# Performance work log

Hardware: AMD Instinct MI355X
Metric: run time of the kernel (lower is better)

Reference implementation:

```python
import jax, jax.numpy as jnp
import numpy as np

D_MODEL = 2048
NUM_HEADS = 16
D_K = D_MODEL // NUM_HEADS
THETA = 10000.0
MAX_SEQ_LEN = 2048
GPT_INIT_STD = 0.02


def setup_inputs() -> dict:
    key = jax.random.key(0)
    ks = jax.random.split(key, 5)
    B, T = 4, 2048
    x = jax.random.normal(ks[0], (B, T, D_MODEL), dtype=jnp.float32)
    token_positions = jnp.arange(T, dtype=jnp.int64 if jax.config.jax_enable_x64 else jnp.int32)[None, :]
    Wq = jax.random.normal(ks[1], (D_MODEL, D_MODEL), dtype=jnp.float32) * GPT_INIT_STD
    Wk = jax.random.normal(ks[2], (D_MODEL, D_MODEL), dtype=jnp.float32) * GPT_INIT_STD
    Wv = jax.random.normal(ks[3], (D_MODEL, D_MODEL), dtype=jnp.float32) * GPT_INIT_STD
    Wo = jax.random.normal(ks[4], (D_MODEL, D_MODEL), dtype=jnp.float32) * GPT_INIT_STD
    return {"x": x, "token_positions": token_positions, "Wq": Wq, "Wk": Wk, "Wv": Wv, "Wo": Wo}


def _rope_tables(dtype):
    # angles[p, j] = p * theta^(-2j/d_k), j in [0, d_k/2)
    j = jnp.arange(D_K // 2, dtype=jnp.float32)
    inv_freq = THETA ** (-2.0 * j / float(D_K))
    pos = jnp.arange(MAX_SEQ_LEN, dtype=jnp.float32)[:, None]
    angles = pos * inv_freq[None, :]
    return jnp.cos(angles).astype(dtype), jnp.sin(angles).astype(dtype)


def _apply_rope(t, cos_pos, sin_pos):
    # t: (b, h, s, d); cos/sin: (1, s, d/2) -> broadcast over (b, h)
    even = t[..., 0::2]
    odd = t[..., 1::2]
    c = cos_pos[:, None, :, :]  # (1,1,s,d/2)
    s = sin_pos[:, None, :, :]
    rot_even = even * c - odd * s
    rot_odd = even * s + odd * c
    out = jnp.stack([rot_even, rot_odd], axis=-1)  # (b,h,s,d/2,2)
    return out.reshape(t.shape)


def reference(x, token_positions, Wq, Wk, Wv, Wo):
    B, T, D = x.shape
    H, d = NUM_HEADS, D_K
    q = (x @ Wq.T).reshape(B, T, H, d).transpose(0, 2, 1, 3)  # (b,h,t,d)
    k = (x @ Wk.T).reshape(B, T, H, d).transpose(0, 2, 1, 3)
    v = (x @ Wv.T).reshape(B, T, H, d).transpose(0, 2, 1, 3)

    cos_tab, sin_tab = _rope_tables(x.dtype)
    cos_pos = cos_tab[token_positions]  # (1, t, d/2)
    sin_pos = sin_tab[token_positions]
    q = _apply_rope(q, cos_pos, sin_pos)
    k = _apply_rope(k, cos_pos, sin_pos)

    # token_positions is strictly increasing and attention_mask is None,
    # so build_attention_mask returns None -> unmasked eager attention.
    scale = float(d) ** -0.5
    scores = jnp.einsum('bhtd,bhsd->bhts', q, k) * scale
    attn = jax.nn.softmax(scores.astype(jnp.float32), axis=-1).astype(q.dtype)
    out = jnp.einsum('bhts,bhsd->bhtd', attn, v)  # (b,h,t,d)
    out = out.transpose(0, 2, 1, 3).reshape(B, T, D)  # (b,t,h*d)
    return out @ Wo.T
```

## Files before the change

kernel.cpp:

```cpp
#include <hip/hip_runtime.h>
#include <hip/hip_bf16.h>
#include <math.h>

#define TSEQ   2048
#define DMODEL 2048
#define NHEAD  16
#define DHEAD  128
#define NBATCH 4
#define MROWS  (NBATCH*TSEQ)

typedef __attribute__((ext_vector_type(8))) short v8s;
typedef __attribute__((ext_vector_type(4))) float v4f;
typedef __attribute__((ext_vector_type(16))) float v16f;

#if __has_builtin(__builtin_amdgcn_exp2f)
#define EXP2(x) __builtin_amdgcn_exp2f(x)
#else
#define EXP2(x) __expf((x) * 0.6931471805599453f)
#endif

__device__ __forceinline__ unsigned short f2b(float f) {
  __hip_bfloat16 h = __float2bfloat16(f);
  return *reinterpret_cast<unsigned short*>(&h);
}
__device__ __forceinline__ unsigned int cvtpk(float lo, float hi) {
  unsigned int r;
  asm("v_cvt_pk_bf16_f32 %0, %1, %2" : "=v"(r) : "v"(lo), "v"(hi));
  return r;
}
__device__ __forceinline__ void gload_lds16(const unsigned short* g, unsigned short* l) {
  __builtin_amdgcn_global_load_lds(
      (const __attribute__((address_space(1))) unsigned int*)g,
      (__attribute__((address_space(3))) unsigned int*)l, 16, 0, 0);
}

__global__ void prep_kernel(const float* __restrict__ x,  const float* __restrict__ Wq,
                            const float* __restrict__ Wk, const float* __restrict__ Wv,
                            const float* __restrict__ Wo, const int* __restrict__ pos,
                            unsigned short* __restrict__ xb,  unsigned short* __restrict__ wqb,
                            unsigned short* __restrict__ wkb, unsigned short* __restrict__ wvb,
                            unsigned short* __restrict__ wob,
                            float* __restrict__ cosT, float* __restrict__ sinT) {
  const int blk = blockIdx.x, tid = threadIdx.x;
  if (blk < 32768) {
    const float* in; unsigned short* out; int lb;
    if      (blk < 16384) { in = x;  out = xb;  lb = blk; }
    else if (blk < 20480) { in = Wq; out = wqb; lb = blk - 16384; }
    else if (blk < 24576) { in = Wk; out = wkb; lb = blk - 20480; }
    else if (blk < 28672) { in = Wv; out = wvb; lb = blk - 24576; }
    else                  { in = Wo; out = wob; lb = blk - 28672; }
    int i = lb * 256 + tid;
    float4 v = reinterpret_cast<const float4*>(in)[i];
    ushort4 o;
    o.x = f2b(v.x); o.y = f2b(v.y); o.z = f2b(v.z); o.w = f2b(v.w);
    reinterpret_cast<ushort4*>(out)[i] = o;
  } else {
    int idx = (blk - 32768) * 256 + tid;
    int t = idx >> 6, j = idx & 63;
    float p = (float)pos[t];
    float inv_freq = expf((-2.0f * (float)j / 128.0f) * logf(10000.0f));
    float ang = p * inv_freq;
    cosT[idx] = cosf(ang);
    sinT[idx] = sinf(ang);
  }
}

template<int MODE>
__global__ __launch_bounds__(512, 2) void gemm8(const unsigned short* __restrict__ A,
                                                const unsigned short* __restrict__ Bt,
                                                void* __restrict__ Cout,
                                                const float* __restrict__ cosT,
                                                const float* __restrict__ sinT) {
  __shared__ unsigned short ldsA[2][256 * 64];
  __shared__ unsigned short ldsB[2][256 * 64];
  const int tid = threadIdx.x;
  const int lane = tid & 63, wv = tid >> 6;
  const int wr = wv >> 2, wc = wv & 3;
  const int g = lane >> 4, r16 = lane & 15;
  const int r7 = r16 & 7;
  const int sl0 = (g ^ r7) << 3;
  const int sl1 = ((4 + g) ^ r7) << 3;

  const int nx = gridDim.x;
  const int nwg = nx * gridDim.y;
  const int lid = blockIdx.y * nx + blockIdx.x;
  const int q8 = nwg >> 3, r8 = nwg & 7;
  const int xcd = lid & 7, off = lid >> 3;
  const int nlid = (xcd < r8 ? xcd * (q8 + 1) : r8 * (q8 + 1) + (xcd - r8) * q8) + off;
  const int mrow0 = (nlid / nx) * 256;
  const int ncol0 = (nlid % nx) * 256;

  const int srow = tid >> 3;
  const int sslot = tid & 7;

  auto stA = [&](int kt, int b, int hf) {
    const int k0 = kt * 64;
#pragma unroll
    for (int j = 0; j < 2; ++j) {
      int r = hf * 128 + j * 64 + srow;
      int slot = sslot ^ (r & 7);
      gload_lds16(&A[(size_t)(mrow0 + r) * DMODEL + k0 + slot * 8],
                  &ldsA[b][(hf * 128 + j * 64) * 64 + tid * 8]);
    }
  };
  auto stB = [&](int kt, int b, int hf) {
    const int k0 = kt * 64;
#pragma unroll
    for (int j = 0; j < 2; ++j) {
      int r = hf * 128 + j * 64 + srow;
      int slot = sslot ^ (r & 7);
      gload_lds16(&Bt[(size_t)(ncol0 + r) * DMODEL + k0 + slot * 8],
                  &ldsB[b][(hf * 128 + j * 64) * 64 + tid * 8]);
    }
  };

  v4f zero = {0.f, 0.f, 0.f, 0.f};
  v4f acc[8][4];
#pragma unroll
  for (int m = 0; m < 8; ++m)
#pragma unroll
    for (int n = 0; n < 4; ++n) acc[m][n] = zero;

  stA(0, 0, 0); stA(0, 0, 1); stB(0, 0, 0); stB(0, 0, 1);
  stA(1, 1, 0); stA(1, 1, 1); stB(1, 1, 0); stB(1, 1, 1);
  asm volatile("s_waitcnt vmcnt(8)" ::: "memory");
  __builtin_amdgcn_s_barrier();

  v8s af[4][2], bf[4][2];
  const int arow = wr * 128 + r16;
  const int brow = wc * 64 + r16;

  for (int kt = 0; kt < DMODEL / 64; ++kt) {
    const int p = kt & 1;
    unsigned short* LA = ldsA[p];
    unsigned short* LB = ldsB[p];

#pragma unroll
    for (int m = 0; m < 4; ++m) {
      af[m][0] = *(const v8s*)&LA[(arow + m * 16) * 64 + sl0];
      af[m][1] = *(const v8s*)&LA[(arow + m * 16) * 64 + sl1];
    }
#pragma unroll
    for (int n = 0; n < 2; ++n) {
      bf[n][0] = *(const v8s*)&LB[(brow + n * 16) * 64 + sl0];
      bf[n][1] = *(const v8s*)&LB[(brow + n * 16) * 64 + sl1];
    }
    __builtin_amdgcn_s_barrier();
    asm volatile("s_waitcnt lgkmcnt(0)" ::: "memory");
    __builtin_amdgcn_sched_barrier(0);
    __builtin_amdgcn_s_setprio(1);
#pragma unroll
    for (int m = 0; m < 4; ++m)
#pragma unroll
      for (int n = 0; n < 2; ++n) {
        acc[m][n] = __builtin_amdgcn_mfma_f32_16x16x32_bf16(af[m][0], bf[n][0], acc[m][n], 0, 0, 0);
        acc[m][n] = __builtin_amdgcn_mfma_f32_16x16x32_bf16(af[m][1], bf[n][1], acc[m][n], 0, 0, 0);
      }
    __builtin_amdgcn_s_setprio(0);
    __builtin_amdgcn_s_barrier();

#pragma unroll
    for (int n = 2; n < 4; ++n) {
      bf[n][0] = *(const v8s*)&LB[(brow + n * 16) * 64 + sl0];
      bf[n][1] = *(const v8s*)&LB[(brow + n * 16) * 64 + sl1];
    }
    __builtin_amdgcn_s_barrier();
    asm volatile("s_waitcnt lgkmcnt(0)" ::: "memory");
    __builtin_amdgcn_sched_barrier(0);
    __builtin_amdgcn_s_setprio(1);
#pragma unroll
    for (int m = 0; m < 4; ++m)
#pragma unroll
      for (int n = 2; n < 4; ++n) {
        acc[m][n] = __builtin_amdgcn_mfma_f32_16x16x32_bf16(af[m][0], bf[n][0], acc[m][n], 0, 0, 0);
        acc[m][n] = __builtin_amdgcn_mfma_f32_16x16x32_bf16(af[m][1], bf[n][1], acc[m][n], 0, 0, 0);
      }
    __builtin_amdgcn_s_setprio(0);
    __builtin_amdgcn_s_barrier();

#pragma unroll
    for (int m = 0; m < 4; ++m) {
      af[m][0] = *(const v8s*)&LA[(arow + 64 + m * 16) * 64 + sl0];
      af[m][1] = *(const v8s*)&LA[(arow + 64 + m * 16) * 64 + sl1];
    }
    if (kt < DMODEL / 64 - 2) { stB(kt + 2, p, 0); stB(kt + 2, p, 1); }
    __builtin_amdgcn_s_barrier();
    asm volatile("s_waitcnt lgkmcnt(0)" ::: "memory");
    __builtin_amdgcn_sched_barrier(0);
    __builtin_amdgcn_s_setprio(1);
#pragma unroll
    for (int m = 0; m < 4; ++m)
#pragma unroll
      for (int n = 2; n < 4; ++n) {
        acc[m + 4][n] = __builtin_amdgcn_mfma_f32_16x16x32_bf16(af[m][0], bf[n][0], acc[m + 4][n], 0, 0, 0);
        acc[m + 4][n] = __builtin_amdgcn_mfma_f32_16x16x32_bf16(af[m][1], bf[n][1], acc[m + 4][n], 0, 0, 0);
      }
    __builtin_amdgcn_s_setprio(0);
    __builtin_amdgcn_s_barrier();

    if (kt < DMODEL / 64 - 2) {
      stA(kt + 2, p, 0); stA(kt + 2, p, 1);
      asm volatile("s_waitcnt vmcnt(8)" ::: "memory");
    } else {
      asm volatile("s_waitcnt vmcnt(0)" ::: "memory");
    }
    __builtin_amdgcn_s_barrier();
    __builtin_amdgcn_s_setprio(1);
#pragma unroll
    for (int m = 0; m < 4; ++m)
#pragma unroll
      for (int n = 0; n < 2; ++n) {
        acc[m + 4][n] = __builtin_amdgcn_mfma_f32_16x16x32_bf16(af[m][0], bf[n][0], acc[m + 4][n], 0, 0, 0);
        acc[m + 4][n] = __builtin_amdgcn_mfma_f32_16x16x32_bf16(af[m][1], bf[n][1], acc[m + 4][n], 0, 0, 0);
      }
    __builtin_amdgcn_s_setprio(0);
    __builtin_amdgcn_s_barrier();
  }

#pragma unroll
  for (int m = 0; m < 8; ++m) {
#pragma unroll
    for (int n = 0; n < 4; ++n) {
#pragma unroll
      for (int r = 0; r < 4; ++r) {
        int row = mrow0 + wr * 128 + m * 16 + g * 4 + r;
        int col = ncol0 + wc * 64 + n * 16 + r16;
        float val = acc[m][n][r];
        if (MODE <= 1) {
          int t = row & (TSEQ - 1), bb = row >> 11;
          int hh = col >> 7, dd = col & (DHEAD - 1);
          float c = cosT[(t << 6) + (dd >> 1)];
          float s = sinT[(t << 6) + (dd >> 1)];
          float pv = __shfl_xor(val, 1);
          float rot = (r16 & 1) ? (pv * s + val * c) : (val * c - pv * s);
          if (MODE == 0) rot *= 0.12751726f;
          ((unsigned short*)Cout)[(((size_t)bb * NHEAD + hh) * TSEQ + t) * DHEAD + dd] = f2b(rot);
        } else if (MODE == 2) {
          int hh = row >> 7, dd = row & (DHEAD - 1);
          int bb = col >> 11, tt = col & (TSEQ - 1);
          ((unsigned short*)Cout)[(((size_t)bb * NHEAD + hh) * DHEAD + dd) * TSEQ + tt] = f2b(val);
        } else {
          ((float*)Cout)[(size_t)row * DMODEL + col] = val;
        }
      }
    }
  }
}

__global__ __launch_bounds__(256, 2) void attn_kernel(const unsigned short* __restrict__ Q,
                                                      const unsigned short* __restrict__ K,
                                                      const unsigned short* __restrict__ Vt,
                                                      unsigned short* __restrict__ O) {
  __shared__ unsigned short Ks[64 * 128];
  __shared__ unsigned short Vs[128 * 64];
  const int tid = threadIdx.x, lane = tid & 63, w = tid >> 6;
  const int hi = lane >> 5, l31 = lane & 31;
  const int bh = blockIdx.y;
  const int b = bh >> 4, h = bh & 15;
  const int qbase = blockIdx.x * 128;
  const size_t hb = (size_t)bh * TSEQ * DHEAD;
  const size_t vb = (size_t)bh * DHEAD * TSEQ;

  v8s qf[8];
  {
    const int qrow = qbase + w * 32 + l31;
#pragma unroll
    for (int dk = 0; dk < 8; ++dk)
      qf[dk] = *(const v8s*)&Q[hb + (size_t)qrow * DHEAD + dk * 16 + hi * 8];
  }

  v16f Z16 = {0,0,0,0,0,0,0,0,0,0,0,0,0,0,0,0};
  v16f o_acc[4];
#pragma unroll
  for (int d = 0; d < 4; ++d) o_acc[d] = Z16;
  float l_run = 0.0f;

  const int ck0 = tid;
  v8s kst[4], vst[4];

#pragma unroll
  for (int hh = 0; hh < 4; ++hh) {
    int ck = ck0 + hh * 256;
    kst[hh] = *(const v8s*)&K[hb + (size_t)(ck >> 4) * DHEAD + (ck & 15) * 8];
    vst[hh] = *(const v8s*)&Vt[vb + (size_t)(ck >> 3) * TSEQ + (ck & 7) * 8];
  }
#pragma unroll
  for (int hh = 0; hh < 4; ++hh) {
    int ck = ck0 + hh * 256;
    int kr = ck >> 4, kc = (ck & 15) * 8;
    *(v8s*)&Ks[kr * 128 + (kc ^ ((kr & 15) << 3))] = kst[hh];
    int vr = ck >> 3, vg = ck & 7;
    *(v8s*)&Vs[vr * 64 + (((vg ^ (vr & 7))) << 3)] = vst[hh];
  }
  __syncthreads();

  for (int s0 = 0; s0 < TSEQ; s0 += 64) {
    const bool last = (s0 + 64 >= TSEQ);
    if (!last) {
#pragma unroll
      for (int hh = 0; hh < 4; ++hh) {
        int ck = ck0 + hh * 256;
        kst[hh] = *(const v8s*)&K[hb + (size_t)(s0 + 64 + (ck >> 4)) * DHEAD + (ck & 15) * 8];
      }
#pragma unroll
      for (int hh = 0; hh < 4; ++hh) {
        int ck = ck0 + hh * 256;
        vst[hh] = *(const v8s*)&Vt[vb + (size_t)(ck >> 3) * TSEQ + s0 + 64 + (ck & 7) * 8];
      }
    }

    v16f s[2]; s[0] = Z16; s[1] = Z16;
    __builtin_amdgcn_s_setprio(1);
#pragma unroll
    for (int kvt = 0; kvt < 2; ++kvt) {
#pragma unroll
      for (int dk = 0; dk < 8; ++dk) {
        int krow = kvt * 32 + l31;
        v8s a = *(const v8s*)&Ks[krow * 128 + ((dk * 16 + hi * 8) ^ ((krow & 15) << 3))];
        s[kvt] = __builtin_amdgcn_mfma_f32_32x32x16_bf16(a, qf[dk], s[kvt], 0, 0, 0);
      }
    }
    __builtin_amdgcn_s_setprio(0);

    __syncthreads();

    if (!last) {
#pragma unroll
      for (int hh = 0; hh < 4; ++hh) {
        int ck = ck0 + hh * 256;
        int kr = ck >> 4, kc = (ck & 15) * 8;
        *(v8s*)&Ks[kr * 128 + (kc ^ ((kr & 15) << 3))] = kst[hh];
      }
    }

    float rowsum = 0.f;
#pragma unroll
    for (int kvt = 0; kvt < 2; ++kvt)
#pragma unroll
      for (int r = 0; r < 16; ++r) {
        float pp = EXP2(s[kvt][r]);
        s[kvt][r] = pp; rowsum += pp;
      }
    l_run += rowsum;

    union { unsigned int u[4]; v8s v; } pf[4];
#pragma unroll
    for (int kvt = 0; kvt < 2; ++kvt) {
      unsigned int wpk[8];
#pragma unroll
      for (int i = 0; i < 8; ++i) wpk[i] = cvtpk(s[kvt][2 * i], s[kvt][2 * i + 1]);
      asm("v_permlane32_swap_b32 %0, %1" : "+v"(wpk[0]), "+v"(wpk[2]));
      asm("v_permlane32_swap_b32 %0, %1" : "+v"(wpk[1]), "+v"(wpk[3]));
      asm("v_permlane32_swap_b32 %0, %1" : "+v"(wpk[4]), "+v"(wpk[6]));
      asm("v_permlane32_swap_b32 %0, %1" : "+v"(wpk[5]), "+v"(wpk[7]));
      pf[2 * kvt].u[0] = wpk[0]; pf[2 * kvt].u[1] = wpk[1];
      pf[2 * kvt].u[2] = wpk[2]; pf[2 * kvt].u[3] = wpk[3];
      pf[2 * kvt + 1].u[0] = wpk[4]; pf[2 * kvt + 1].u[1] = wpk[5];
      pf[2 * kvt + 1].u[2] = wpk[6]; pf[2 * kvt + 1].u[3] = wpk[7];
    }

    __builtin_amdgcn_s_setprio(1);
#pragma unroll
    for (int kvt = 0; kvt < 2; ++kvt) {
      const int g0 = kvt * 4 + hi;
#pragma unroll
      for (int d = 0; d < 4; ++d) {
        int drow = d * 32 + l31;
        int sx = drow & 7;
        v8s vf0 = *(const v8s*)&Vs[drow * 64 + (((g0    ) ^ sx) << 3)];
        v8s vf1 = *(const v8s*)&Vs[drow * 64 + (((g0 + 2) ^ sx) << 3)];
        o_acc[d] = __builtin_amdgcn_mfma_f32_32x32x16_bf16(pf[2 * kvt].v, vf0, o_acc[d], 0, 0, 0);
        o_acc[d] = __builtin_amdgcn_mfma_f32_32x32x16_bf16(pf[2 * kvt + 1].v, vf1, o_acc[d], 0, 0, 0);
      }
    }
    __builtin_amdgcn_s_setprio(0);

    __syncthreads();

    if (!last) {
#pragma unroll
      for (int hh = 0; hh < 4; ++hh) {
        int ck = ck0 + hh * 256;
        int vr = ck >> 3, vg = ck & 7;
        *(v8s*)&Vs[vr * 64 + (((vg ^ (vr & 7))) << 3)] = vst[hh];
      }
    }
  }

#pragma unroll
  for (int r = 0; r < 16; ++r) {
    int qi = (r & 3) + 8 * (r >> 2) + 4 * hi;
    float lq = __shfl(l_run, qi) + __shfl(l_run, qi + 32);
    float inv = 1.0f / lq;
    int t = qbase + w * 32 + qi;
#pragma unroll
    for (int d = 0; d < 4; ++d) {
      O[((size_t)(b * TSEQ + t)) * DMODEL + h * DHEAD + d * 32 + l31] = f2b(o_acc[d][r] * inv);
    }
  }
}

extern "C" void kernel_launch(void* const* d_in, const int* in_sizes, int n_in,
                              void* d_out, int out_size, void* d_ws, size_t ws_size,
                              hipStream_t stream) {
  const float* x  = (const float*)d_in[0];
  const int*   pos = (const int*)d_in[1];
  const float* Wq = (const float*)d_in[2];
  const float* Wk = (const float*)d_in[3];
  const float* Wv = (const float*)d_in[4];
  const float* Wo = (const float*)d_in[5];
  float* out = (float*)d_out;
  char* ws = (char*)d_ws;

  const size_t WBYTES = (size_t)DMODEL * DMODEL * 2;
  const size_t XBYTES = (size_t)MROWS * DMODEL * 2;
  unsigned short* wqb = (unsigned short*)(ws);
  unsigned short* wkb = (unsigned short*)(ws + WBYTES);
  unsigned short* wvb = (unsigned short*)(ws + 2 * WBYTES);
  unsigned short* wob = (unsigned short*)(ws + 3 * WBYTES);
  unsigned short* xb  = (unsigned short*)(ws + 4 * WBYTES);
  unsigned short* Qb  = (unsigned short*)(ws + 4 * WBYTES + XBYTES);
  unsigned short* Kb  = (unsigned short*)(ws + 4 * WBYTES + 2 * XBYTES);
  unsigned short* Vtb = (unsigned short*)(ws + 4 * WBYTES + 3 * XBYTES);
  float* cosT = (float*)(ws + 4 * WBYTES + 4 * XBYTES);
  float* sinT = cosT + TSEQ * 64;
  if (ws_size < 4 * WBYTES + 4 * XBYTES + 2 * (size_t)TSEQ * 64 * sizeof(float)) return;

  prep_kernel<<<33280, 256, 0, stream>>>(x, Wq, Wk, Wv, Wo, pos,
                                         xb, wqb, wkb, wvb, wob, cosT, sinT);

  dim3 gg(DMODEL / 256, MROWS / 256);
  gemm8<0><<<gg, 512, 0, stream>>>(xb, wqb, (void*)Qb, cosT, sinT);
  gemm8<1><<<gg, 512, 0, stream>>>(xb, wkb, (void*)Kb, cosT, sinT);
  gemm8<2><<<dim3(MROWS / 256, DMODEL / 256), 512, 0, stream>>>(wvb, xb, (void*)Vtb, cosT, sinT);

  attn_kernel<<<dim3(TSEQ / 128, 64), 256, 0, stream>>>(Qb, Kb, Vtb, xb);

  gemm8<3><<<gg, 512, 0, stream>>>(xb, wob, (void*)out, cosT, sinT);
}
```

Before: 485.1 us.

## Pack RoPE cos/sin as fp16 pairs and reswizzle V tile in attention LDS

The RoPE tables are now stored as one interleaved half2 word per (position, frequency) instead of two separate float arrays, so the projection epilogue does a single 4-byte load per element. This lowers epilogue memory traffic but reduces cos/sin precision to fp16. Separately, the V tile in the attention kernel's LDS is laid out as 128-wide rows, two d-rows per row, with a 16-way XOR swizzle. The aim is to cut LDS bank conflicts on the V fragment reads feeding the MFMAs.

```diff
diff --git a/kernel.cpp b/kernel.cpp
--- a/kernel.cpp
+++ b/kernel.cpp
@@ -1,5 +1,6 @@
 #include <hip/hip_runtime.h>
 #include <hip/hip_bf16.h>
+#include <hip/hip_fp16.h>
 #include <math.h>
 
 #define TSEQ   2048
@@ -40,7 +41,7 @@
                             unsigned short* __restrict__ xb,  unsigned short* __restrict__ wqb,
                             unsigned short* __restrict__ wkb, unsigned short* __restrict__ wvb,
                             unsigned short* __restrict__ wob,
-                            float* __restrict__ cosT, float* __restrict__ sinT) {
+                            unsigned int* __restrict__ ropeT) {
   const int blk = blockIdx.x, tid = threadIdx.x;
   if (blk < 32768) {
     const float* in; unsigned short* out; int lb;
@@ -60,8 +61,8 @@
     float p = (float)pos[t];
     float inv_freq = expf((-2.0f * (float)j / 128.0f) * logf(10000.0f));
     float ang = p * inv_freq;
-    cosT[idx] = cosf(ang);
-    sinT[idx] = sinf(ang);
+    __half2 h2 = __floats2half2_rn(cosf(ang), sinf(ang));
+    ropeT[idx] = *reinterpret_cast<unsigned int*>(&h2);
   }
 }
 
@@ -69,8 +70,7 @@
 __global__ __launch_bounds__(512, 2) void gemm8(const unsigned short* __restrict__ A,
                                                 const unsigned short* __restrict__ Bt,
                                                 void* __restrict__ Cout,
-                                                const float* __restrict__ cosT,
-                                                const float* __restrict__ sinT) {
+                                                const unsigned int* __restrict__ ropeT) {
   __shared__ unsigned short ldsA[2][256 * 64];
   __shared__ unsigned short ldsB[2][256 * 64];
   const int tid = threadIdx.x;
@@ -229,8 +229,10 @@
         if (MODE <= 1) {
           int t = row & (TSEQ - 1), bb = row >> 11;
           int hh = col >> 7, dd = col & (DHEAD - 1);
-          float c = cosT[(t << 6) + (dd >> 1)];
-          float s = sinT[(t << 6) + (dd >> 1)];
+          unsigned int csu = ropeT[(t << 6) + (dd >> 1)];
+          __half2 h2 = *reinterpret_cast<__half2*>(&csu);
+          float c = __half2float(__low2half(h2));
+          float s = __half2float(__high2half(h2));
           float pv = __shfl_xor(val, 1);
           float rot = (r16 & 1) ? (pv * s + val * c) : (val * c - pv * s);
           if (MODE == 0) rot *= 0.12751726f;
@@ -252,7 +254,7 @@
                                                       const unsigned short* __restrict__ Vt,
                                                       unsigned short* __restrict__ O) {
   __shared__ unsigned short Ks[64 * 128];
-  __shared__ unsigned short Vs[128 * 64];
+  __shared__ unsigned short Vs[64 * 128];
   const int tid = threadIdx.x, lane = tid & 63, w = tid >> 6;
   const int hi = lane >> 5, l31 = lane & 31;
   const int bh = blockIdx.y;
@@ -290,7 +292,8 @@
     int kr = ck >> 4, kc = (ck & 15) * 8;
     *(v8s*)&Ks[kr * 128 + (kc ^ ((kr & 15) << 3))] = kst[hh];
     int vr = ck >> 3, vg = ck & 7;
-    *(v8s*)&Vs[vr * 64 + (((vg ^ (vr & 7))) << 3)] = vst[hh];
+    int slot = (((vr & 1) << 3) | vg) ^ ((vr >> 1) & 15);
+    *(v8s*)&Vs[(vr >> 1) * 128 + slot * 8] = vst[hh];
   }
   __syncthreads();
 
@@ -366,9 +369,11 @@
 #pragma unroll
       for (int d = 0; d < 4; ++d) {
         int drow = d * 32 + l31;
-        int sx = drow & 7;
-        v8s vf0 = *(const v8s*)&Vs[drow * 64 + (((g0    ) ^ sx) << 3)];
-        v8s vf1 = *(const v8s*)&Vs[drow * 64 + (((g0 + 2) ^ sx) << 3)];
+        int lr = drow >> 1;
+        int x = (drow & 1) << 3;
+        int sw = lr & 15;
+        v8s vf0 = *(const v8s*)&Vs[lr * 128 + (((x | g0) ^ sw) << 3)];
+        v8s vf1 = *(const v8s*)&Vs[lr * 128 + (((x | (g0 + 2)) ^ sw) << 3)];
         o_acc[d] = __builtin_amdgcn_mfma_f32_32x32x16_bf16(pf[2 * kvt].v, vf0, o_acc[d], 0, 0, 0);
         o_acc[d] = __builtin_amdgcn_mfma_f32_32x32x16_bf16(pf[2 * kvt + 1].v, vf1, o_acc[d], 0, 0, 0);
       }
@@ -382,7 +387,8 @@
       for (int hh = 0; hh < 4; ++hh) {
         int ck = ck0 + hh * 256;
         int vr = ck >> 3, vg = ck & 7;
-        *(v8s*)&Vs[vr * 64 + (((vg ^ (vr & 7))) << 3)] = vst[hh];
+        int slot = (((vr & 1) << 3) | vg) ^ ((vr >> 1) & 15);
+        *(v8s*)&Vs[(vr >> 1) * 128 + slot * 8] = vst[hh];
       }
     }
   }
@@ -422,19 +428,18 @@
   unsigned short* Qb  = (unsigned short*)(ws + 4 * WBYTES + XBYTES);
   unsigned short* Kb  = (unsigned short*)(ws + 4 * WBYTES + 2 * XBYTES);
   unsigned short* Vtb = (unsigned short*)(ws + 4 * WBYTES + 3 * XBYTES);
-  float* cosT = (float*)(ws + 4 * WBYTES + 4 * XBYTES);
-  float* sinT = cosT + TSEQ * 64;
-  if (ws_size < 4 * WBYTES + 4 * XBYTES + 2 * (size_t)TSEQ * 64 * sizeof(float)) return;
+  unsigned int* ropeT = (unsigned int*)(ws + 4 * WBYTES + 4 * XBYTES);
+  if (ws_size < 4 * WBYTES + 4 * XBYTES + (size_t)TSEQ * 64 * sizeof(unsigned int)) return;
 
   prep_kernel<<<33280, 256, 0, stream>>>(x, Wq, Wk, Wv, Wo, pos,
-                                         xb, wqb, wkb, wvb, wob, cosT, sinT);
+                                         xb, wqb, wkb, wvb, wob, ropeT);
 
   dim3 gg(DMODEL / 256, MROWS / 256);
-  gemm8<0><<<gg, 512, 0, stream>>>(xb, wqb, (void*)Qb, cosT, sinT);
-  gemm8<1><<<gg, 512, 0, stream>>>(xb, wkb, (void*)Kb, cosT, sinT);
-  gemm8<2><<<dim3(MROWS / 256, DMODEL / 256), 512, 0, stream>>>(wvb, xb, (void*)Vtb, cosT, sinT);
+  gemm8<0><<<gg, 512, 0, stream>>>(xb, wqb, (void*)Qb, ropeT);
+  gemm8<1><<<gg, 512, 0, stream>>>(xb, wkb, (void*)Kb, ropeT);
+  gemm8<2><<<dim3(MROWS / 256, DMODEL / 256), 512, 0, stream>>>(wvb, xb, (void*)Vtb, ropeT);
 
   attn_kernel<<<dim3(TSEQ / 128, 64), 256, 0, stream>>>(Qb, Kb, Vtb, xb);
 
-  gemm8<3><<<gg, 512, 0, stream>>>(xb, wob, (void*)out, cosT, sinT);
-}
+  gemm8<3><<<gg, 512, 0, stream>>>(xb, wob, (void*)out, ropeT);
+}
```

Result: no change. 480.2 us (-1.0%).
